# Performance work log

Hardware: AMD Instinct MI355X
Metric: run time of the kernel (lower is better)

## Reference

```python
import jax, jax.numpy as jnp
import numpy as np

KH = KW = 3
PAD = 1
OFFG = 8  # offset groups: 144 offset channels / (2*9)


def conv2d(x, w, b, pad=PAD):
    out = jax.lax.conv_general_dilated(
        x, w, window_strides=(1, 1), padding=[(pad, pad), (pad, pad)],
        dimension_numbers=('NCHW', 'OIHW', 'NCHW'))
    return out + b[None, :, None, None]


def deform_conv2d(x, offset, w, b):
    # x: [B,C,H,W], offset: [B, 2*K*OFFG, H, W] (per group: (y,x) per kernel tap)
    B, C, H, W = x.shape
    K = KH * KW
    Cg = C // OFFG
    off = offset.reshape(B, OFFG, K, 2, H, W)
    ky, kx = jnp.meshgrid(jnp.arange(KH), jnp.arange(KW), indexing='ij')
    ky = ky.reshape(K).astype(x.dtype)
    kx = kx.reshape(K).astype(x.dtype)
    ys = (jnp.arange(H) - PAD).astype(x.dtype)  # stride 1, dilation 1
    xs = (jnp.arange(W) - PAD).astype(x.dtype)
    # sampling positions [B, OFFG, K, H, W]
    py = ys[None, None, None, :, None] + ky[None, None, :, None, None] + off[:, :, :, 0]
    px = xs[None, None, None, None, :] + kx[None, None, :, None, None] + off[:, :, :, 1]
    y0 = jnp.floor(py)
    x0 = jnp.floor(px)
    xg = x.reshape(B, OFFG, Cg, H * W)
    cols = jnp.zeros((B, OFFG, Cg, K, H, W), x.dtype)
    for dy in (0, 1):
        for dx in (0, 1):
            yi = y0 + dy
            xi = x0 + dx
            wgt = (1.0 - jnp.abs(py - yi)) * (1.0 - jnp.abs(px - xi))
            valid = (yi >= 0) & (yi < H) & (xi >= 0) & (xi < W)
            yc = jnp.clip(yi, 0, H - 1).astype(jnp.int32)
            xc = jnp.clip(xi, 0, W - 1).astype(jnp.int32)
            idx = (yc * W + xc).reshape(B, OFFG, 1, K * H * W)
            g = jnp.take_along_axis(xg, idx, axis=3).reshape(B, OFFG, Cg, K, H, W)
            cols = cols + g * (wgt * valid.astype(x.dtype))[:, :, None]
    cols = cols.reshape(B, C, K, H, W)
    out = jnp.einsum('bckhw,ock->bohw', cols, w.reshape(w.shape[0], C, K))
    return out + b[None, :, None, None]


def setup_inputs() -> dict:
    key = jax.random.key(0)
    ks = jax.random.split(key, 6)
    B, C, H, W = 16, 144, 64, 64
    feat_arm = jax.random.normal(ks[0], (B, C, H, W), jnp.float32)
    feat_up = jax.random.normal(ks[1], (B, C, H, W), jnp.float32)
    # offset conv: in=288 (cat), out=144 = 2*9*OFFG; small init so offsets are sane
    off_w = jax.random.normal(ks[2], (144, 288, 3, 3), jnp.float32) * 0.01
    off_b = jnp.zeros((144,), jnp.float32)
    dcn_w = jax.random.normal(ks[3], (256, 144, 3, 3), jnp.float32) * (1.0 / np.sqrt(144 * 9))
    dcn_b = jnp.zeros((256,), jnp.float32)
    return {'feat_arm': feat_arm, 'feat_up': feat_up, 'off_w': off_w,
            'off_b': off_b, 'dcn_w': dcn_w, 'dcn_b': dcn_b}


def reference(feat_arm, feat_up, off_w, off_b, dcn_w, dcn_b):
    x = jnp.concatenate([feat_arm, feat_up], axis=1)  # [B, 288, H, W]
    offset = conv2d(x, off_w, off_b)                  # [B, 144, H, W]
    y = deform_conv2d(feat_up, offset, dcn_w, dcn_b)  # [B, 256, H, W]
    return jax.nn.silu(y)
```

## Files before the change

kernel.cpp:

```cpp
#include <hip/hip_runtime.h>
#include <math.h>

constexpr int BN = 16;
constexpr int C_IN = 144, C_CAT = 288, C_OFF = 144, C_OUT = 256;
constexpr int OFFG = 8, CG = 18;

constexpr int FUB_ELEMS  = C_IN * BN * 4096;
constexpr int OFFP_ELEMS = BN * 72 * 4096;
constexpr int WOFF_PACK = 9 * 9 * 9 * 512;
constexpr int WDCN_PACK = 8 * 6 * 16 * 512;

typedef __attribute__((ext_vector_type(8))) short bf16x8;
typedef __attribute__((ext_vector_type(8))) _Float16 f16x8;
typedef __attribute__((ext_vector_type(2))) _Float16 f16x2;
typedef __attribute__((ext_vector_type(4))) float f32x4;
typedef __attribute__((ext_vector_type(4))) unsigned u32x4;

__device__ __forceinline__ unsigned short f2bf(float f) {
  unsigned u = __builtin_bit_cast(unsigned, f);
  return (unsigned short)((u + 0x7FFFu + ((u >> 16) & 1u)) >> 16);
}

__device__ __forceinline__ unsigned packh2(float a, float b) {
  unsigned short ha = __builtin_bit_cast(unsigned short, (_Float16)a);
  unsigned short hb = __builtin_bit_cast(unsigned short, (_Float16)b);
  return (unsigned)ha | ((unsigned)hb << 16);
}
__device__ __forceinline__ float h2f_lo(unsigned u) {
  return (float)__builtin_bit_cast(_Float16, (unsigned short)(u & 0xFFFFu));
}
__device__ __forceinline__ float h2f_hi(unsigned u) {
  return (float)__builtin_bit_cast(_Float16, (unsigned short)(u >> 16));
}

__device__ __forceinline__ void gload_lds16(const void* g, void* l) {
  __builtin_amdgcn_global_load_lds(
      (const __attribute__((address_space(1))) unsigned*)g,
      (__attribute__((address_space(3))) unsigned*)l, 16, 0, 0);
}

__global__ __launch_bounds__(256) void prep(
    const float* __restrict__ off_w, const float* __restrict__ dcn_w,
    unsigned short* __restrict__ wo, _Float16* __restrict__ wd) {
  int idx = blockIdx.x * 256 + threadIdx.x;
  if (idx < WOFF_PACK) {
    int i = idx & 7, lane = (idx >> 3) & 63, t = idx >> 9;
    int mt = t % 9; t /= 9;
    int tap = t % 9, cb = t / 9;
    int co = mt * 16 + (lane & 15);
    int ci = cb * 32 + ((lane >> 4) << 3) + i;
    wo[idx] = f2bf(off_w[(co * C_CAT + ci) * 9 + tap]);
  }
  if (idx < WDCN_PACK) {
    int i = idx & 7, lane = (idx >> 3) & 63, t = idx >> 9;
    int mt = t & 15; t >>= 4;
    int ks = t % 6, g = t / 6;
    int co = mt * 16 + (lane & 15);
    int r = ks * 32 + ((lane >> 4) << 3) + i;
    float v = 0.f;
    if (r < 162) {
      int ci = r / 9, tap = r - ci * 9;
      v = dcn_w[(co * C_IN + g * CG + ci) * 9 + tap];
    }
    wd[idx] = (_Float16)v;
  }
}

__global__ __launch_bounds__(256) void offs_conv_mfma(
    const float* __restrict__ fa, const float* __restrict__ fu,
    const unsigned short* __restrict__ wt, const float* __restrict__ bias,
    unsigned* __restrict__ offp, _Float16* __restrict__ fuB) {
  const int bid = (blockIdx.x & 7) * 64 + (blockIdx.x >> 3);
  const int b = bid >> 5;
  const int y0 = (bid & 31) << 1;
  const int tid = threadIdx.x;
  const int wave = tid >> 6, lane = tid & 63;
  const int kg = lane >> 4, ln = lane & 15;

  __shared__ __align__(16) unsigned short xs[4 * 66 * 32];

  f32x4 acc[9][2];
#pragma unroll
  for (int m = 0; m < 9; ++m)
#pragma unroll
    for (int n = 0; n < 2; ++n) acc[m][n] = {0.f, 0.f, 0.f, 0.f};

  for (int cb = 0; cb < 9; ++cb) {
    __syncthreads();
    for (int idx = tid; idx < 2112; idx += 256) {
      int q = idx / 264;
      int rem = idx - q * 264;
      int row = rem / 66;
      int cc = rem - row * 66;
      int y = y0 - 1 + row, x = cc - 1;
      ushort4 wv = make_ushort4(0, 0, 0, 0);
      if (y >= 0 && y < 64 && x >= 0 && x < 64) {
        int cib = cb * 32 + (q << 2);
        const float* p = (cib < C_IN)
                             ? fa + (((size_t)(b * C_IN + cib)) << 12)
                             : fu + (((size_t)(b * C_IN + cib - C_IN)) << 12);
        int o = (y << 6) + x;
        float v0 = p[o], v1 = p[o + 4096], v2 = p[o + 8192], v3 = p[o + 12288];
        wv.x = f2bf(v0);
        wv.y = f2bf(v1);
        wv.z = f2bf(v2);
        wv.w = f2bf(v3);
        if (cib >= C_IN && row >= 1 && row <= 2) {
          _Float16* fb = fuB + (((size_t)(b * C_IN + cib - C_IN)) << 12) + o;
          fb[0] = (_Float16)v0;
          fb[4096] = (_Float16)v1;
          fb[8192] = (_Float16)v2;
          fb[12288] = (_Float16)v3;
        }
      }
      int e = ((row * 66 + cc) << 5) + (((q >> 1) ^ (cc & 3)) << 3) + ((q & 1) << 2);
      *(ushort4*)&xs[e] = wv;
    }
    __syncthreads();

    for (int tap = 0; tap < 9; ++tap) {
      const int ky = tap / 3, kx = tap - ky * 3;
      bf16x8 a[9];
      const unsigned short* wp = wt + (((size_t)(cb * 9 + tap) * 9) << 9) + (lane << 3);
#pragma unroll
      for (int m = 0; m < 9; ++m) a[m] = *(const bf16x8*)(wp + (m << 9));
#pragma unroll
      for (int n = 0; n < 2; ++n) {
        int px = ((wave << 1) + n) * 16 + ln;
        int row = (px >> 6) + ky, cc = (px & 63) + kx;
        int e = ((row * 66 + cc) << 5) + ((kg ^ (cc & 3)) << 3);
        bf16x8 bv = *(const bf16x8*)&xs[e];
        __builtin_amdgcn_s_setprio(1);
#pragma unroll
        for (int m = 0; m < 9; ++m)
          acc[m][n] = __builtin_amdgcn_mfma_f32_16x16x32_bf16(a[m], bv, acc[m][n], 0, 0, 0);
        __builtin_amdgcn_s_setprio(0);
      }
    }
  }

#pragma unroll
  for (int n = 0; n < 2; ++n) {
    int px = ((wave << 1) + n) * 16 + ln;
    int y = y0 + (px >> 6), x = px & 63;
#pragma unroll
    for (int m = 0; m < 9; ++m) {
      int cob = m * 16 + (kg << 2);
#pragma unroll
      for (int rr = 0; rr < 4; rr += 2) {
        unsigned v = packh2(acc[m][n][rr] + bias[cob + rr],
                            acc[m][n][rr + 1] + bias[cob + rr + 1]);
        offp[(((size_t)(b * 72 + ((cob + rr) >> 1))) << 12) + (y << 6) + x] = v;
      }
    }
  }
}

__global__ __launch_bounds__(512, 4) void dcn_mfma(
    const _Float16* __restrict__ fuB, const unsigned* __restrict__ offp,
    const _Float16* __restrict__ wt, const float* __restrict__ bias,
    float* __restrict__ out) {
  const int bid = (blockIdx.x & 7) * 128 + (blockIdx.x >> 3);
  const int b = bid >> 6, h = bid & 63;
  const int tid = threadIdx.x;
  const int wave = tid >> 6, lane = tid & 63;
  const int kg = lane >> 4, ln = lane & 15;
  const int wm = wave >> 2, wn = wave & 3;
  const int px = (wn << 4) + ln;

  __shared__ __align__(16) unsigned short colsT[64 * 202];
  __shared__ __align__(16) _Float16 wl[3][8192];

  f32x4 acc[8];
#pragma unroll
  for (int m = 0; m < 8; ++m) acc[m] = {0.f, 0.f, 0.f, 0.f};

  for (int i = tid; i < 64 * 15; i += 512) {
    int p = i / 15, d = i - p * 15;
    *(unsigned*)&colsT[p * 202 + 162 + 2 * d] = 0u;
  }

  {
    const _Float16* src = wt + (wave * 2) * 512 + lane * 8;
#pragma unroll
    for (int j = 0; j < 2; ++j)
      gload_lds16(src + j * 512, &wl[0][(wave * 2 + j) * 512]);
  }

  auto make_geo = [&](int gg_, int tap, int p) -> uint4 {
    int ky = tap / 3, kx = tap - ky * 3;
    unsigned op = offp[(((size_t)(b * 72 + gg_ * 9 + tap)) << 12) + (h << 6) + p];
    float oy = h2f_lo(op), ox = h2f_hi(op);
    float py = (float)(h - 1 + ky) + oy;
    float pxs = (float)(p - 1 + kx) + ox;
    float y0f = floorf(py), x0f = floorf(pxs);
    int y0 = (int)y0f, x0 = (int)x0f;
    float fy = py - y0f, fx = pxs - x0f;
    float vy0 = (y0 >= 0 && y0 < 64) ? 1.f : 0.f;
    float vy1 = (y0 + 1 >= 0 && y0 + 1 < 64) ? 1.f : 0.f;
    float vx0 = (x0 >= 0 && x0 < 64) ? 1.f : 0.f;
    float vx1 = (x0 + 1 >= 0 && x0 + 1 < 64) ? 1.f : 0.f;
    float a0 = (1.f - fx) * vx0;
    float a1 = fx * vx1;
    float wlo = (x0 == -1) ? a1 : (x0 == 63 ? 0.f : a0);
    float whi = (x0 == 63) ? a0 : (x0 == -1 ? 0.f : a1);
    int xL = min(max(x0, 0), 62);
    int yc0 = min(max(y0, 0), 63), yc1 = min(max(y0 + 1, 0), 63);
    float cy0 = (1.f - fy) * vy0, cy1 = fy * vy1;
    uint4 r;
    r.x = (unsigned)((yc0 << 6) + xL) | ((unsigned)((yc1 << 6) + xL) << 16);
    r.y = 0u;
    r.z = packh2(cy0 * wlo, cy0 * whi);
    r.w = packh2(cy1 * wlo, cy1 * whi);
    return r;
  };

  int tg = 0, cur = 0;
  for (int g = 0; g < OFFG; ++g) {
    __syncthreads();

    uint4 gg = make_geo(g, wave, lane);
    uint4 g8 = make_geo(g, 8, lane);

    const _Float16* gbase = fuB + (((size_t)(b * C_IN + g * CG)) << 12);
    {
      const int iL0 = gg.x & 0xFFFFu, iL1 = gg.x >> 16;
      const f16x2 w0 = __builtin_bit_cast(f16x2, gg.z);
      const f16x2 w1 = __builtin_bit_cast(f16x2, gg.w);
      const int j0 = g8.x & 0xFFFFu, j1 = g8.x >> 16;
      const f16x2 u0 = __builtin_bit_cast(f16x2, g8.z);
      const f16x2 u1 = __builtin_bit_cast(f16x2, g8.w);
      const int n8 = (wave < 2) ? 3 : 2;

      unsigned d0[18], d1[18], e0[3], e1[3];
#pragma unroll
      for (int u = 0; u < 18; ++u) {
        const _Float16* pl = gbase + ((size_t)u << 12);
        __builtin_memcpy(&d0[u], pl + iL0, 4);
        __builtin_memcpy(&d1[u], pl + iL1, 4);
      }
#pragma unroll
      for (int u = 0; u < 3; ++u) {
        if (u < n8) {
          const _Float16* pl = gbase + ((size_t)(wave + 8 * u) << 12);
          __builtin_memcpy(&e0[u], pl + j0, 4);
          __builtin_memcpy(&e1[u], pl + j1, 4);
        }
      }
#pragma unroll
      for (int u = 0; u < 18; ++u) {
        f16x2 sp = __builtin_bit_cast(f16x2, d0[u]) * w0 +
                   __builtin_bit_cast(f16x2, d1[u]) * w1;
        _Float16 s = sp[0] + sp[1];
        colsT[lane * 202 + u * 9 + wave] = __builtin_bit_cast(unsigned short, s);
      }
#pragma unroll
      for (int u = 0; u < 3; ++u) {
        if (u < n8) {
          f16x2 sp = __builtin_bit_cast(f16x2, e0[u]) * u0 +
                     __builtin_bit_cast(f16x2, e1[u]) * u1;
          _Float16 s = sp[0] + sp[1];
          colsT[lane * 202 + (wave + 8 * u) * 9 + 8] =
              __builtin_bit_cast(unsigned short, s);
        }
      }
    }
    __syncthreads();

    for (int ks = 0; ks < 6; ++ks, ++tg) {
      int cbase = px * 202 + ks * 32 + (kg << 3);
      u32x4 bu;
      bu[0] = *(const unsigned*)&colsT[cbase];
      bu[1] = *(const unsigned*)&colsT[cbase + 2];
      bu[2] = *(const unsigned*)&colsT[cbase + 4];
      bu[3] = *(const unsigned*)&colsT[cbase + 6];
      f16x8 bv = __builtin_bit_cast(f16x8, bu);

      int nxt = cur + 1;
      if (nxt == 3) nxt = 0;
      if (tg < 47) {
        const _Float16* src =
            wt + (size_t)(tg + 1) * 8192 + (wave * 2) * 512 + lane * 8;
        _Float16* dst = wl[nxt];
#pragma unroll
        for (int j = 0; j < 2; ++j)
          gload_lds16(src + j * 512, dst + (wave * 2 + j) * 512);
        asm volatile("s_waitcnt vmcnt(2)" ::: "memory");
      } else {
        asm volatile("s_waitcnt vmcnt(0)" ::: "memory");
      }
      __builtin_amdgcn_s_barrier();

      const _Float16* wbuf = wl[cur] + (wm * 8) * 512 + lane * 8;
      __builtin_amdgcn_s_setprio(1);
#pragma unroll
      for (int j = 0; j < 8; ++j) {
        f16x8 av = *(const f16x8*)(wbuf + j * 512);
        acc[j] = __builtin_amdgcn_mfma_f32_16x16x32_f16(av, bv, acc[j], 0, 0, 0);
      }
      __builtin_amdgcn_s_setprio(0);
      cur = nxt;
    }
  }

#pragma unroll
  for (int j = 0; j < 8; ++j) {
    int cob = (wm * 8 + j) * 16 + (kg << 2);
#pragma unroll
    for (int r = 0; r < 4; ++r) {
      float y = acc[j][r] + bias[cob + r];
      out[(((size_t)(b * C_OUT + cob + r)) << 12) + (h << 6) + px] =
          y / (1.f + expf(-y));
    }
  }
}

extern "C" void kernel_launch(void* const* d_in, const int* in_sizes, int n_in,
                              void* d_out, int out_size, void* d_ws, size_t ws_size,
                              hipStream_t stream) {
  const float* feat_arm = (const float*)d_in[0];
  const float* feat_up  = (const float*)d_in[1];
  const float* off_w    = (const float*)d_in[2];
  const float* off_b    = (const float*)d_in[3];
  const float* dcn_w    = (const float*)d_in[4];
  const float* dcn_b    = (const float*)d_in[5];
  float* out = (float*)d_out;

  _Float16* fuB = (_Float16*)d_ws;
  unsigned* offp = (unsigned*)(fuB + FUB_ELEMS);
  unsigned short* wo = (unsigned short*)(offp + OFFP_ELEMS);
  _Float16* wd = (_Float16*)(wo + WOFF_PACK);

  prep<<<(WDCN_PACK + 255) / 256, 256, 0, stream>>>(off_w, dcn_w, wo, wd);
  offs_conv_mfma<<<BN * 32, 256, 0, stream>>>(feat_arm, feat_up, wo, off_b, offp, fuB);
  dcn_mfma<<<BN * 64, 512, 0, stream>>>(fuB, offp, wd, dcn_b, out);
}
```

Measured before the change: 248.4 us.

## Load DCN weight fragments directly from global into registers, dropping LDS staging

```diff
diff --git a/kernel.cpp b/kernel.cpp
--- a/kernel.cpp
+++ b/kernel.cpp
@@ -31,12 +31,6 @@
 }
 __device__ __forceinline__ float h2f_hi(unsigned u) {
   return (float)__builtin_bit_cast(_Float16, (unsigned short)(u >> 16));
-}
-
-__device__ __forceinline__ void gload_lds16(const void* g, void* l) {
-  __builtin_amdgcn_global_load_lds(
-      (const __attribute__((address_space(1))) unsigned*)g,
-      (__attribute__((address_space(3))) unsigned*)l, 16, 0, 0);
 }
 
 __global__ __launch_bounds__(256) void prep(
@@ -169,7 +163,6 @@
   const int px = (wn << 4) + ln;
 
   __shared__ __align__(16) unsigned short colsT[64 * 202];
-  __shared__ __align__(16) _Float16 wl[3][8192];
 
   f32x4 acc[8];
 #pragma unroll
@@ -178,13 +171,6 @@
   for (int i = tid; i < 64 * 15; i += 512) {
     int p = i / 15, d = i - p * 15;
     *(unsigned*)&colsT[p * 202 + 162 + 2 * d] = 0u;
-  }
-
-  {
-    const _Float16* src = wt + (wave * 2) * 512 + lane * 8;
-#pragma unroll
-    for (int j = 0; j < 2; ++j)
-      gload_lds16(src + j * 512, &wl[0][(wave * 2 + j) * 512]);
   }
 
   auto make_geo = [&](int gg_, int tap, int p) -> uint4 {
@@ -215,7 +201,6 @@
     return r;
   };
 
-  int tg = 0, cur = 0;
   for (int g = 0; g < OFFG; ++g) {
     __syncthreads();
 
@@ -267,7 +252,28 @@
     }
     __syncthreads();
 
-    for (int ks = 0; ks < 6; ++ks, ++tg) {
+    for (int ks = 0; ks < 6; ++ks) {
+      const _Float16* wpA =
+          wt + (size_t)(g * 6 + ks) * 8192 + (wm * 8) * 512 + (size_t)lane * 8;
+      const _Float16* wpB = wpA + 2048;
+      u32x4 r0, r1, r2, r3, r4, r5, r6, r7;
+      asm volatile("global_load_dwordx4 %0, %1, off offset:0"
+                   : "=v"(r0) : "v"(wpA));
+      asm volatile("global_load_dwordx4 %0, %1, off offset:1024"
+                   : "=v"(r1) : "v"(wpA));
+      asm volatile("global_load_dwordx4 %0, %1, off offset:2048"
+                   : "=v"(r2) : "v"(wpA));
+      asm volatile("global_load_dwordx4 %0, %1, off offset:3072"
+                   : "=v"(r3) : "v"(wpA));
+      asm volatile("global_load_dwordx4 %0, %1, off offset:0"
+                   : "=v"(r4) : "v"(wpB));
+      asm volatile("global_load_dwordx4 %0, %1, off offset:1024"
+                   : "=v"(r5) : "v"(wpB));
+      asm volatile("global_load_dwordx4 %0, %1, off offset:2048"
+                   : "=v"(r6) : "v"(wpB));
+      asm volatile("global_load_dwordx4 %0, %1, off offset:3072"
+                   : "=v"(r7) : "v"(wpB));
+
       int cbase = px * 202 + ks * 32 + (kg << 3);
       u32x4 bu;
       bu[0] = *(const unsigned*)&colsT[cbase];
@@ -276,30 +282,27 @@
       bu[3] = *(const unsigned*)&colsT[cbase + 6];
       f16x8 bv = __builtin_bit_cast(f16x8, bu);
 
-      int nxt = cur + 1;
-      if (nxt == 3) nxt = 0;
-      if (tg < 47) {
-        const _Float16* src =
-            wt + (size_t)(tg + 1) * 8192 + (wave * 2) * 512 + lane * 8;
-        _Float16* dst = wl[nxt];
-#pragma unroll
-        for (int j = 0; j < 2; ++j)
-          gload_lds16(src + j * 512, dst + (wave * 2 + j) * 512);
-        asm volatile("s_waitcnt vmcnt(2)" ::: "memory");
-      } else {
-        asm volatile("s_waitcnt vmcnt(0)" ::: "memory");
-      }
-      __builtin_amdgcn_s_barrier();
-
-      const _Float16* wbuf = wl[cur] + (wm * 8) * 512 + lane * 8;
+      asm volatile("s_waitcnt vmcnt(0)" ::: "memory");
+      __builtin_amdgcn_sched_barrier(0);
+
       __builtin_amdgcn_s_setprio(1);
-#pragma unroll
-      for (int j = 0; j < 8; ++j) {
-        f16x8 av = *(const f16x8*)(wbuf + j * 512);
-        acc[j] = __builtin_amdgcn_mfma_f32_16x16x32_f16(av, bv, acc[j], 0, 0, 0);
-      }
+      acc[0] = __builtin_amdgcn_mfma_f32_16x16x32_f16(
+          __builtin_bit_cast(f16x8, r0), bv, acc[0], 0, 0, 0);
+      acc[1] = __builtin_amdgcn_mfma_f32_16x16x32_f16(
+          __builtin_bit_cast(f16x8, r1), bv, acc[1], 0, 0, 0);
+      acc[2] = __builtin_amdgcn_mfma_f32_16x16x32_f16(
+          __builtin_bit_cast(f16x8, r2), bv, acc[2], 0, 0, 0);
+      acc[3] = __builtin_amdgcn_mfma_f32_16x16x32_f16(
+          __builtin_bit_cast(f16x8, r3), bv, acc[3], 0, 0, 0);
+      acc[4] = __builtin_amdgcn_mfma_f32_16x16x32_f16(
+          __builtin_bit_cast(f16x8, r4), bv, acc[4], 0, 0, 0);
+      acc[5] = __builtin_amdgcn_mfma_f32_16x16x32_f16(
+          __builtin_bit_cast(f16x8, r5), bv, acc[5], 0, 0, 0);
+      acc[6] = __builtin_amdgcn_mfma_f32_16x16x32_f16(
+          __builtin_bit_cast(f16x8, r6), bv, acc[6], 0, 0, 0);
+      acc[7] = __builtin_amdgcn_mfma_f32_16x16x32_f16(
+          __builtin_bit_cast(f16x8, r7), bv, acc[7], 0, 0, 0);
       __builtin_amdgcn_s_setprio(0);
-      cur = nxt;
     }
   }
 
```

Measured after the change: 294.9 us. 18.7% more time.
